# Kernel optimization log

Hardware: AMD Instinct MI355X
Metric: run time of the kernel (lower is better)

## Reference

```python
import jax, jax.numpy as jnp
import numpy as np

TMP = 5.0  # temperature from init kwarg tmp=5

def _l2norm(x, axis, eps=1e-12):
    n = jnp.linalg.norm(x, axis=axis, keepdims=True)
    return x / jnp.maximum(n, eps)

def setup_inputs() -> dict:
    key = jax.random.key(0)
    ks = jax.random.split(key, 6)
    B, C, A, D, H = 128, 200, 312, 2048, 1600
    return {
        "AttM": jax.random.uniform(ks[0], (C, A), dtype=jnp.float32),
        "x_in": jax.random.uniform(ks[1], (B, D), dtype=jnp.float32),
        "Wg": jax.random.normal(ks[2], (A, D), dtype=jnp.float32) * 0.02,
        "bg": jnp.zeros((A,), jnp.float32),
        "W1": jax.random.normal(ks[3], (H, A), dtype=jnp.float32) * 0.02,
        "b1": jnp.zeros((H,), jnp.float32),
        "W2": jax.random.normal(ks[4], (D, H), dtype=jnp.float32) * 0.02,
        "b2": jnp.zeros((D,), jnp.float32),
        "bias_p": jnp.zeros((1,), jnp.float32),
        "scale_cls": jnp.full((1,), 10.0, jnp.float32),
    }

def reference(AttM, x_in, Wg, bg, W1, b1, W2, b2, bias_p, scale_cls):
    # x = F.normalize(input)  (p=2, dim=1)
    x = _l2norm(x_in, 1)                                   # [B, D]
    # attention over attribute dims from image features
    att = jax.nn.relu(x @ Wg.T + bg)                        # [B, A]
    att = jax.nn.softmax(att / TMP, axis=1)                 # [B, A]
    att = att[:, None, :] + 1.0                             # [B, 1, A] (att + ones)
    comb = att * AttM[None, :, :]                           # [B, C, A]
    # per-(sample,class) generated classifier via 2-layer MLP
    h = jax.nn.relu(jnp.einsum('bca,ha->bch', comb, W1) + b1)     # [B, C, 1600]
    cls = jax.nn.relu(jnp.einsum('bch,dh->bcd', h, W2) + b2)      # [B, C, D]
    cls = _l2norm(cls, -1)
    # original: matmul(classifier, x.T) -> [B,C,B], permute+diagonal -> [B,C].
    # Only the per-sample diagonal is kept, which equals a direct dot product:
    out = scale_cls[0] * (jnp.einsum('bcd,bd->bc', cls, x) + bias_p[0])  # [B, C]
    return out
```

## Files before the change

kernel.cpp:

```cpp
#include <hip/hip_runtime.h>
#include <hip/hip_bf16.h>
#include <math.h>

#define BB 128
#define CC 200
#define AA 312
#define AAP 320
#define DD 2048
#define HH 1600
#define HHP 1664
#define MM 25600

typedef __attribute__((ext_vector_type(8))) short bf16x8;
typedef __attribute__((ext_vector_type(4))) float f32x4;

__device__ __forceinline__ unsigned short f2bf(float f) {
  union { float f; unsigned int u; } v; v.f = f;
  unsigned int u = v.u;
  unsigned int r = (u + 0x7fffu + ((u >> 16) & 1u)) >> 16;
  return (unsigned short)r;
}
__device__ __forceinline__ float bf2f(unsigned short b) {
  union { unsigned int u; float f; } v; v.u = ((unsigned int)b) << 16;
  return v.f;
}

__device__ __forceinline__ void gload_lds16(const void* g, void* l) {
  __builtin_amdgcn_global_load_lds(
      (const __attribute__((address_space(1))) unsigned int*)g,
      (__attribute__((address_space(3))) unsigned int*)l, 16, 0, 0);
}

__global__ __launch_bounds__(256)
void k_norm_attn(const float* __restrict__ x_in, const unsigned short* __restrict__ Wgb,
                 const float* __restrict__ bg, float* __restrict__ xf,
                 float* __restrict__ attp) {
  int b = blockIdx.x;
  int t = threadIdx.x, wv = t >> 6, ln = t & 63;
  __shared__ float xs[DD];
  __shared__ float sa[AA];
  __shared__ float wsum[4];
  const float4* xi = (const float4*)(x_in + (size_t)b * DD);
  float4 v0 = xi[t], v1 = xi[t + 256];
  float s = v0.x*v0.x + v0.y*v0.y + v0.z*v0.z + v0.w*v0.w
          + v1.x*v1.x + v1.y*v1.y + v1.z*v1.z + v1.w*v1.w;
  for (int off = 32; off; off >>= 1) s += __shfl_xor(s, off, 64);
  if (ln == 0) wsum[wv] = s;
  __syncthreads();
  float sc = 1.f / fmaxf(sqrtf(wsum[0] + wsum[1] + wsum[2] + wsum[3]), 1e-12f);
  v0.x *= sc; v0.y *= sc; v0.z *= sc; v0.w *= sc;
  v1.x *= sc; v1.y *= sc; v1.z *= sc; v1.w *= sc;
  float4* xo = (float4*)(xf + (size_t)b * DD);
  xo[t] = v0; xo[t + 256] = v1;
  ((float4*)xs)[t] = v0; ((float4*)xs)[t + 256] = v1;
  __syncthreads();
  for (int a = wv; a < AA; a += 4) {
    const bf16x8* wrow = (const bf16x8*)(Wgb + (size_t)a * DD);
    float acc = 0.f;
#pragma unroll
    for (int j = 0; j < 4; j++) {
      bf16x8 w = wrow[j * 64 + ln];
      const float* xv = &xs[(j * 64 + ln) * 8];
#pragma unroll
      for (int e = 0; e < 8; e++) acc += bf2f((unsigned short)w[e]) * xv[e];
    }
    for (int off = 32; off; off >>= 1) acc += __shfl_xor(acc, off, 64);
    if (ln == 0) sa[a] = fmaxf(acc + bg[a], 0.f) * 0.2f;
  }
  __syncthreads();
  if (wv == 0) {
    float mx = -1e30f;
    for (int i = ln; i < AA; i += 64) mx = fmaxf(mx, sa[i]);
    for (int off = 32; off; off >>= 1) mx = fmaxf(mx, __shfl_xor(mx, off, 64));
    float ev[5]; float sm = 0.f;
#pragma unroll
    for (int k = 0; k < 5; k++) {
      int i = ln + k * 64;
      ev[k] = (i < AA) ? expf(sa[i] - mx) : 0.f;
      sm += ev[k];
    }
    for (int off = 32; off; off >>= 1) sm += __shfl_xor(sm, off, 64);
    float inv = 1.f / sm;
#pragma unroll
    for (int k = 0; k < 5; k++) {
      int i = ln + k * 64;
      if (i < AA) attp[(size_t)b * AA + i] = 1.f + ev[k] * inv;
    }
  }
}

__global__ void k_comb(const float* __restrict__ attp, const float* __restrict__ AttM,
                       unsigned short* __restrict__ comb) {
  int m = blockIdx.x;
  int a = threadIdx.x;
  int b = m / CC, c = m % CC;
  unsigned short v = 0;
  if (a < AA) v = f2bf(attp[(size_t)b * AA + a] * AttM[(size_t)c * AA + a]);
  comb[(size_t)m * AAP + a] = v;
}

#define R1SZ (HHP * AAP)
#define R2SZ (DD * HHP)
#define R3SZ (AA * DD)
__global__ void k_cast_all(const float* __restrict__ W1, const float* __restrict__ W2,
                           const float* __restrict__ Wg, unsigned short* __restrict__ W1b,
                           unsigned short* __restrict__ W2b, unsigned short* __restrict__ Wgb) {
  int i = blockIdx.x * 256 + threadIdx.x;
  if (i < R1SZ) {
    int r = i / AAP, c = i % AAP;
    W1b[i] = (r < HH && c < AA) ? f2bf(W1[(size_t)r * AA + c]) : (unsigned short)0;
  } else if (i < R1SZ + R2SZ) {
    int j = i - R1SZ;
    int r = j / HHP, c = j % HHP;
    W2b[j] = (c < HH) ? f2bf(W2[(size_t)r * HH + c]) : (unsigned short)0;
  } else if (i < R1SZ + R2SZ + R3SZ) {
    int j = i - R1SZ - R2SZ;
    Wgb[j] = f2bf(Wg[j]);
  }
}

template <int KD, int NT>
__device__ __forceinline__ void gemm_core(const unsigned short* __restrict__ A,
                                          const unsigned short* __restrict__ Bm,
                                          short* As, short* Bs, f32x4 (&acc)[4][4],
                                          size_t ar0, size_t br0, int tid, int w, int ln) {
  const int scol = (((tid & 7) ^ ((tid >> 3) & 7)) << 3);
  const unsigned short* aP = A + (ar0 + (tid >> 3)) * KD + scol;
  const unsigned short* bP = Bm + (br0 + (tid >> 3)) * KD + scol;
  const int lr = ln & 15, hi = ln >> 4;
  const int axor0 = ((hi ^ (lr & 7)) << 3);
  const int axor1 = (((4 + hi) ^ (lr & 7)) << 3);
  const int wrow = (w >> 1) * 64, wcol = (w & 1) * 64;
  const int abase = (wrow + lr) * 64, bbase = (wcol + lr) * 64;
  for (int kt = 0; kt < NT; ++kt) {
#pragma unroll
    for (int p = 0; p < 4; p++) {
      gload_lds16(aP + (size_t)(p * 32) * KD + kt * 64, &As[p * 2048 + tid * 8]);
      gload_lds16(bP + (size_t)(p * 32) * KD + kt * 64, &Bs[p * 2048 + tid * 8]);
    }
    __syncthreads();
    bf16x8 av[4][2], bv[4][2];
#pragma unroll
    for (int i = 0; i < 4; i++) {
      av[i][0] = *(const bf16x8*)&As[abase + i * 1024 + axor0];
      av[i][1] = *(const bf16x8*)&As[abase + i * 1024 + axor1];
    }
#pragma unroll
    for (int i = 0; i < 4; i++) {
      bv[i][0] = *(const bf16x8*)&Bs[bbase + i * 1024 + axor0];
      bv[i][1] = *(const bf16x8*)&Bs[bbase + i * 1024 + axor1];
    }
#pragma unroll
    for (int m = 0; m < 4; m++)
#pragma unroll
      for (int n = 0; n < 4; n++) {
        acc[m][n] = __builtin_amdgcn_mfma_f32_16x16x32_bf16(av[m][0], bv[n][0], acc[m][n], 0, 0, 0);
        acc[m][n] = __builtin_amdgcn_mfma_f32_16x16x32_bf16(av[m][1], bv[n][1], acc[m][n], 0, 0, 0);
      }
    __syncthreads();
  }
}

__global__ __launch_bounds__(256, 4)
void k_gemm_h(const unsigned short* __restrict__ A, const unsigned short* __restrict__ Bm,
              const float* __restrict__ bias, unsigned short* __restrict__ C) {
  __shared__ short As[128 * 64];
  __shared__ short Bs[128 * 64];
  int tid = threadIdx.x, w = tid >> 6, ln = tid & 63;
  f32x4 acc[4][4] = {};
  gemm_core<AAP, AAP / 64>(A, Bm, As, Bs, acc, (size_t)blockIdx.y * 128,
                           (size_t)blockIdx.x * 128, tid, w, ln);
  int wrow = (w >> 1) * 64, wcol = (w & 1) * 64;
  int gr0 = blockIdx.y * 128 + wrow + (ln >> 4) * 4;
  int gc0 = blockIdx.x * 128 + wcol + (ln & 15);
#pragma unroll
  for (int m = 0; m < 4; m++)
#pragma unroll
    for (int r = 0; r < 4; r++) {
      size_t grow = (size_t)(gr0 + m * 16 + r);
#pragma unroll
      for (int n = 0; n < 4; n++) {
        int gcol = gc0 + n * 16;
        float v = acc[m][n][r] + (gcol < HH ? bias[gcol] : 0.f);
        C[grow * HHP + gcol] = f2bf(fmaxf(v, 0.f));
      }
    }
}

__global__ __launch_bounds__(256, 4)
void k_gemm_cls(const unsigned short* __restrict__ A, const unsigned short* __restrict__ Bm,
                const float* __restrict__ b2, const float* __restrict__ xf,
                float* __restrict__ dotb, float* __restrict__ nrm2b) {
  __shared__ short As[128 * 64];
  __shared__ short Bs[128 * 64];
  int tid = threadIdx.x, w = tid >> 6, ln = tid & 63;
  f32x4 acc[4][4] = {};
  gemm_core<HHP, HHP / 64>(A, Bm, As, Bs, acc, (size_t)blockIdx.y * 128,
                           (size_t)blockIdx.x * 128, tid, w, ln);
  int wrow = (w >> 1) * 64, wcol = (w & 1) * 64;
  int gr0 = blockIdx.y * 128 + wrow + (ln >> 4) * 4;
  int gc0 = blockIdx.x * 128 + wcol + (ln & 15);
  float bias[4];
#pragma unroll
  for (int n = 0; n < 4; n++) bias[n] = b2[gc0 + n * 16];
#pragma unroll
  for (int m = 0; m < 4; m++)
#pragma unroll
    for (int r = 0; r < 4; r++) {
      int grow = gr0 + m * 16 + r;
      int b = grow / CC;
      const float* xr = xf + (size_t)b * DD;
      float s1 = 0.f, s2 = 0.f;
#pragma unroll
      for (int n = 0; n < 4; n++) {
        float cls = fmaxf(acc[m][n][r] + bias[n], 0.f);
        s1 += cls * cls;
        s2 += cls * xr[gc0 + n * 16];
      }
      s1 += __shfl_xor(s1, 1, 64); s2 += __shfl_xor(s2, 1, 64);
      s1 += __shfl_xor(s1, 2, 64); s2 += __shfl_xor(s2, 2, 64);
      s1 += __shfl_xor(s1, 4, 64); s2 += __shfl_xor(s2, 4, 64);
      s1 += __shfl_xor(s1, 8, 64); s2 += __shfl_xor(s2, 8, 64);
      if ((ln & 15) == 0) {
        atomicAdd(&nrm2b[grow], s1);
        atomicAdd(&dotb[grow], s2);
      }
    }
}

__global__ void k_final(const float* __restrict__ dotb, const float* __restrict__ nrm2b,
                        const float* __restrict__ bias_p, const float* __restrict__ scale_cls,
                        float* __restrict__ out) {
  int i = blockIdx.x * 256 + threadIdx.x;
  if (i < MM)
    out[i] = scale_cls[0] * (dotb[i] / fmaxf(sqrtf(nrm2b[i]), 1e-12f) + bias_p[0]);
}

extern "C" void kernel_launch(void* const* d_in, const int* in_sizes, int n_in,
                              void* d_out, int out_size, void* d_ws, size_t ws_size,
                              hipStream_t stream) {
  const float* AttM = (const float*)d_in[0];
  const float* x_in = (const float*)d_in[1];
  const float* Wg = (const float*)d_in[2];
  const float* bg = (const float*)d_in[3];
  const float* W1 = (const float*)d_in[4];
  const float* b1 = (const float*)d_in[5];
  const float* W2 = (const float*)d_in[6];
  const float* b2 = (const float*)d_in[7];
  const float* bias_p = (const float*)d_in[8];
  const float* scale_cls = (const float*)d_in[9];
  float* out = (float*)d_out;

  char* ws = (char*)d_ws;
  size_t off = 0;
  auto alloc = [&](size_t bytes) {
    char* p = ws + off;
    off += (bytes + 255) & ~(size_t)255;
    return p;
  };
  float* xf = (float*)alloc((size_t)BB * DD * 4);
  float* attp = (float*)alloc((size_t)BB * AA * 4);
  unsigned short* comb = (unsigned short*)alloc((size_t)MM * AAP * 2);
  unsigned short* W1b = (unsigned short*)alloc((size_t)HHP * AAP * 2);
  unsigned short* W2b = (unsigned short*)alloc((size_t)DD * HHP * 2);
  unsigned short* Wgb = (unsigned short*)alloc((size_t)AA * DD * 2);
  unsigned short* hbuf = (unsigned short*)alloc((size_t)MM * HHP * 2);
  float* dotb = (float*)alloc((size_t)MM * 4);
  float* nrm2b = (float*)alloc((size_t)MM * 4);
  (void)ws_size; (void)in_sizes; (void)n_in; (void)out_size;

  hipMemsetAsync(dotb, 0, (size_t)MM * 4 * 2, stream);

  k_cast_all<<<(R1SZ + R2SZ + R3SZ + 255) / 256, 256, 0, stream>>>(W1, W2, Wg, W1b, W2b, Wgb);
  k_norm_attn<<<BB, 256, 0, stream>>>(x_in, Wgb, bg, xf, attp);
  k_comb<<<MM, AAP, 0, stream>>>(attp, AttM, comb);
  k_gemm_h<<<dim3(HHP / 128, MM / 128), 256, 0, stream>>>(comb, W1b, b1, hbuf);
  k_gemm_cls<<<dim3(DD / 128, MM / 128), 256, 0, stream>>>(hbuf, W2b, b2, xf, dotb, nrm2b);
  k_final<<<(MM + 255) / 256, 256, 0, stream>>>(dotb, nrm2b, bias_p, scale_cls, out);
}
```

Measured before the change: 327.9 us.

## Fuse comb into attention kernel, unpad hidden dim, vectorize casts, swizzle GEMM blocks

Folds the comb construction into the normalization/attention kernel, so the separate 25600-block launch and the attp round trip go away. The hidden dimension is stored unpadded at 1600 instead of 1664, which cuts the second GEMM's K loop from 26 to 25 tiles and shrinks hbuf and W2b. The weight cast kernel now handles four elements per thread with float4 loads. Both GEMMs remap block IDs to group work across XCDs for better L2 reuse. The risk is that the 1600 row stride may misalign the LDS-swizzled loads, and the remainder handling of the 128-wide tiles for H is now implicit.

```diff
diff --git a/kernel.cpp b/kernel.cpp
--- a/kernel.cpp
+++ b/kernel.cpp
@@ -13,6 +13,7 @@
 
 typedef __attribute__((ext_vector_type(8))) short bf16x8;
 typedef __attribute__((ext_vector_type(4))) float f32x4;
+typedef __attribute__((ext_vector_type(4))) unsigned short u16x4;
 
 __device__ __forceinline__ unsigned short f2bf(float f) {
   union { float f; unsigned int u; } v; v.f = f;
@@ -33,13 +34,14 @@
 
 __global__ __launch_bounds__(256)
 void k_norm_attn(const float* __restrict__ x_in, const unsigned short* __restrict__ Wgb,
-                 const float* __restrict__ bg, float* __restrict__ xf,
-                 float* __restrict__ attp) {
+                 const float* __restrict__ bg, const float* __restrict__ AttM,
+                 float* __restrict__ xf, unsigned short* __restrict__ comb) {
   int b = blockIdx.x;
   int t = threadIdx.x, wv = t >> 6, ln = t & 63;
   __shared__ float xs[DD];
-  __shared__ float sa[AA];
+  __shared__ float satt[AAP];
   __shared__ float wsum[4];
+  if (t < AAP - AA) satt[AA + t] = 0.f;
   const float4* xi = (const float4*)(x_in + (size_t)b * DD);
   float4 v0 = xi[t], v1 = xi[t + 256];
   float s = v0.x*v0.x + v0.y*v0.y + v0.z*v0.z + v0.w*v0.w
@@ -65,18 +67,18 @@
       for (int e = 0; e < 8; e++) acc += bf2f((unsigned short)w[e]) * xv[e];
     }
     for (int off = 32; off; off >>= 1) acc += __shfl_xor(acc, off, 64);
-    if (ln == 0) sa[a] = fmaxf(acc + bg[a], 0.f) * 0.2f;
+    if (ln == 0) satt[a] = fmaxf(acc + bg[a], 0.f) * 0.2f;
   }
   __syncthreads();
   if (wv == 0) {
     float mx = -1e30f;
-    for (int i = ln; i < AA; i += 64) mx = fmaxf(mx, sa[i]);
+    for (int i = ln; i < AA; i += 64) mx = fmaxf(mx, satt[i]);
     for (int off = 32; off; off >>= 1) mx = fmaxf(mx, __shfl_xor(mx, off, 64));
     float ev[5]; float sm = 0.f;
 #pragma unroll
     for (int k = 0; k < 5; k++) {
       int i = ln + k * 64;
-      ev[k] = (i < AA) ? expf(sa[i] - mx) : 0.f;
+      ev[k] = (i < AA) ? expf(satt[i] - mx) : 0.f;
       sm += ev[k];
     }
     for (int off = 32; off; off >>= 1) sm += __shfl_xor(sm, off, 64);
@@ -84,38 +86,52 @@
 #pragma unroll
     for (int k = 0; k < 5; k++) {
       int i = ln + k * 64;
-      if (i < AA) attp[(size_t)b * AA + i] = 1.f + ev[k] * inv;
-    }
-  }
-}
-
-__global__ void k_comb(const float* __restrict__ attp, const float* __restrict__ AttM,
-                       unsigned short* __restrict__ comb) {
-  int m = blockIdx.x;
-  int a = threadIdx.x;
-  int b = m / CC, c = m % CC;
-  unsigned short v = 0;
-  if (a < AA) v = f2bf(attp[(size_t)b * AA + a] * AttM[(size_t)c * AA + a]);
-  comb[(size_t)m * AAP + a] = v;
+      if (i < AA) satt[i] = 1.f + ev[k] * inv;
+    }
+  }
+  __syncthreads();
+  const size_t mbase = (size_t)b * CC;
+  for (int idx = t; idx < CC * 40; idx += 256) {
+    int c = idx / 40, j = idx - c * 40;
+    bf16x8 v = {};
+    if (j < 39) {
+      const float4* ap = (const float4*)(AttM + (size_t)c * AA + j * 8);
+      float4 p0 = ap[0], p1 = ap[1];
+      const float* sv = &satt[j * 8];
+      v[0] = (short)f2bf(p0.x * sv[0]); v[1] = (short)f2bf(p0.y * sv[1]);
+      v[2] = (short)f2bf(p0.z * sv[2]); v[3] = (short)f2bf(p0.w * sv[3]);
+      v[4] = (short)f2bf(p1.x * sv[4]); v[5] = (short)f2bf(p1.y * sv[5]);
+      v[6] = (short)f2bf(p1.z * sv[6]); v[7] = (short)f2bf(p1.w * sv[7]);
+    }
+    *(bf16x8*)(comb + (mbase + c) * AAP + j * 8) = v;
+  }
 }
 
 #define R1SZ (HHP * AAP)
-#define R2SZ (DD * HHP)
+#define R2SZ (DD * HH)
 #define R3SZ (AA * DD)
 __global__ void k_cast_all(const float* __restrict__ W1, const float* __restrict__ W2,
                            const float* __restrict__ Wg, unsigned short* __restrict__ W1b,
                            unsigned short* __restrict__ W2b, unsigned short* __restrict__ Wgb) {
-  int i = blockIdx.x * 256 + threadIdx.x;
+  int i = (blockIdx.x * 256 + threadIdx.x) * 4;
   if (i < R1SZ) {
-    int r = i / AAP, c = i % AAP;
-    W1b[i] = (r < HH && c < AA) ? f2bf(W1[(size_t)r * AA + c]) : (unsigned short)0;
+    int r = i / AAP, c = i - r * AAP;
+    u16x4 o = {};
+    if (r < HH && c < AA) {
+      float4 f = *(const float4*)(W1 + (size_t)r * AA + c);
+      o[0] = f2bf(f.x); o[1] = f2bf(f.y); o[2] = f2bf(f.z); o[3] = f2bf(f.w);
+    }
+    *(u16x4*)(W1b + i) = o;
   } else if (i < R1SZ + R2SZ) {
     int j = i - R1SZ;
-    int r = j / HHP, c = j % HHP;
-    W2b[j] = (c < HH) ? f2bf(W2[(size_t)r * HH + c]) : (unsigned short)0;
+    float4 f = *(const float4*)(W2 + j);
+    u16x4 o; o[0] = f2bf(f.x); o[1] = f2bf(f.y); o[2] = f2bf(f.z); o[3] = f2bf(f.w);
+    *(u16x4*)(W2b + j) = o;
   } else if (i < R1SZ + R2SZ + R3SZ) {
     int j = i - R1SZ - R2SZ;
-    Wgb[j] = f2bf(Wg[j]);
+    float4 f = *(const float4*)(Wg + j);
+    u16x4 o; o[0] = f2bf(f.x); o[1] = f2bf(f.y); o[2] = f2bf(f.z); o[3] = f2bf(f.w);
+    *(u16x4*)(Wgb + j) = o;
   }
 }
 
@@ -167,12 +183,15 @@
   __shared__ short As[128 * 64];
   __shared__ short Bs[128 * 64];
   int tid = threadIdx.x, w = tid >> 6, ln = tid & 63;
+  int bid = blockIdx.x + blockIdx.y * gridDim.x;
+  int lid = (bid & 7) * 325 + (bid >> 3);
+  int bx = lid % 13, by = lid / 13;
   f32x4 acc[4][4] = {};
-  gemm_core<AAP, AAP / 64>(A, Bm, As, Bs, acc, (size_t)blockIdx.y * 128,
-                           (size_t)blockIdx.x * 128, tid, w, ln);
+  gemm_core<AAP, AAP / 64>(A, Bm, As, Bs, acc, (size_t)by * 128,
+                           (size_t)bx * 128, tid, w, ln);
   int wrow = (w >> 1) * 64, wcol = (w & 1) * 64;
-  int gr0 = blockIdx.y * 128 + wrow + (ln >> 4) * 4;
-  int gc0 = blockIdx.x * 128 + wcol + (ln & 15);
+  int gr0 = by * 128 + wrow + (ln >> 4) * 4;
+  int gc0 = bx * 128 + wcol + (ln & 15);
 #pragma unroll
   for (int m = 0; m < 4; m++)
 #pragma unroll
@@ -181,8 +200,10 @@
 #pragma unroll
       for (int n = 0; n < 4; n++) {
         int gcol = gc0 + n * 16;
-        float v = acc[m][n][r] + (gcol < HH ? bias[gcol] : 0.f);
-        C[grow * HHP + gcol] = f2bf(fmaxf(v, 0.f));
+        if (gcol < HH) {
+          float v = acc[m][n][r] + bias[gcol];
+          C[grow * HH + gcol] = f2bf(fmaxf(v, 0.f));
+        }
       }
     }
 }
@@ -194,12 +215,15 @@
   __shared__ short As[128 * 64];
   __shared__ short Bs[128 * 64];
   int tid = threadIdx.x, w = tid >> 6, ln = tid & 63;
+  int bid = blockIdx.x + blockIdx.y * gridDim.x;
+  int lid = (bid & 7) * 400 + (bid >> 3);
+  int bx = lid & 15, by = lid >> 4;
   f32x4 acc[4][4] = {};
-  gemm_core<HHP, HHP / 64>(A, Bm, As, Bs, acc, (size_t)blockIdx.y * 128,
-                           (size_t)blockIdx.x * 128, tid, w, ln);
+  gemm_core<HH, HH / 64>(A, Bm, As, Bs, acc, (size_t)by * 128,
+                         (size_t)bx * 128, tid, w, ln);
   int wrow = (w >> 1) * 64, wcol = (w & 1) * 64;
-  int gr0 = blockIdx.y * 128 + wrow + (ln >> 4) * 4;
-  int gc0 = blockIdx.x * 128 + wcol + (ln & 15);
+  int gr0 = by * 128 + wrow + (ln >> 4) * 4;
+  int gc0 = bx * 128 + wcol + (ln & 15);
   float bias[4];
 #pragma unroll
   for (int n = 0; n < 4; n++) bias[n] = b2[gc0 + n * 16];
@@ -259,22 +283,20 @@
     return p;
   };
   float* xf = (float*)alloc((size_t)BB * DD * 4);
-  float* attp = (float*)alloc((size_t)BB * AA * 4);
   unsigned short* comb = (unsigned short*)alloc((size_t)MM * AAP * 2);
-  unsigned short* W1b = (unsigned short*)alloc((size_t)HHP * AAP * 2);
-  unsigned short* W2b = (unsigned short*)alloc((size_t)DD * HHP * 2);
-  unsigned short* Wgb = (unsigned short*)alloc((size_t)AA * DD * 2);
-  unsigned short* hbuf = (unsigned short*)alloc((size_t)MM * HHP * 2);
+  unsigned short* W1b = (unsigned short*)alloc((size_t)R1SZ * 2);
+  unsigned short* W2b = (unsigned short*)alloc((size_t)R2SZ * 2);
+  unsigned short* Wgb = (unsigned short*)alloc((size_t)R3SZ * 2);
+  unsigned short* hbuf = (unsigned short*)alloc((size_t)MM * HH * 2);
   float* dotb = (float*)alloc((size_t)MM * 4);
   float* nrm2b = (float*)alloc((size_t)MM * 4);
   (void)ws_size; (void)in_sizes; (void)n_in; (void)out_size;
 
   hipMemsetAsync(dotb, 0, (size_t)MM * 4 * 2, stream);
 
-  k_cast_all<<<(R1SZ + R2SZ + R3SZ + 255) / 256, 256, 0, stream>>>(W1, W2, Wg, W1b, W2b, Wgb);
-  k_norm_attn<<<BB, 256, 0, stream>>>(x_in, Wgb, bg, xf, attp);
-  k_comb<<<MM, AAP, 0, stream>>>(attp, AttM, comb);
-  k_gemm_h<<<dim3(HHP / 128, MM / 128), 256, 0, stream>>>(comb, W1b, b1, hbuf);
+  k_cast_all<<<((R1SZ + R2SZ + R3SZ) / 4 + 255) / 256, 256, 0, stream>>>(W1, W2, Wg, W1b, W2b, Wgb);
+  k_norm_attn<<<BB, 256, 0, stream>>>(x_in, Wgb, bg, AttM, xf, comb);
+  k_gemm_h<<<dim3(13, MM / 128), 256, 0, stream>>>(comb, W1b, b1, hbuf);
   k_gemm_cls<<<dim3(DD / 128, MM / 128), 256, 0, stream>>>(hbuf, W2b, b2, xf, dotb, nrm2b);
   k_final<<<(MM + 255) / 256, 256, 0, stream>>>(dotb, nrm2b, bias_p, scale_cls, out);
 }
```

New measurement: 315.4 us. -3.8%, faster.
